# Optimization experiments

Measured on AMD Instinct MI355X. Metric: run time of the kernel, lower is better.

The kernel has to match this reference:

```python
import jax, jax.numpy as jnp
import numpy as np

VOCAB = 50000
D_EMB = 300
N_BINS = 11
B, LQ, LD = 64, 32, 1024
MU = np.array([1.0, 0.9, 0.7, 0.5, 0.3, 0.1, -0.1, -0.3, -0.5, -0.7, -0.9], dtype=np.float32)
SIGMA = np.array([1e-3] + [0.1] * 10, dtype=np.float32)


def setup_inputs() -> dict:
    key = jax.random.key(0)
    ks = jax.random.split(key, 8)
    inputs_q = jax.random.randint(ks[0], (B, LQ), 0, VOCAB, dtype=jnp.int64 if jax.config.jax_enable_x64 else jnp.int32)
    inputs_d = jax.random.randint(ks[1], (B, LD), 0, VOCAB, dtype=jnp.int64 if jax.config.jax_enable_x64 else jnp.int32)
    mask_q = jnp.ones((B, LQ), dtype=jnp.float32)
    mask_d = jnp.ones((B, LD), dtype=jnp.float32)
    word_emb = jax.random.normal(ks[2], (VOCAB, D_EMB), dtype=jnp.float32) * 0.1
    attn_table = jax.random.uniform(ks[3], (VOCAB, 1), dtype=jnp.float32)  # frozen IDF embedding
    idf_w = jax.random.normal(ks[4], (1, 1), dtype=jnp.float32)
    idf_b = jnp.zeros((1,), dtype=jnp.float32)
    dense_w = jax.random.normal(ks[5], (1, N_BINS), dtype=jnp.float32) * 0.1
    dense_b = jnp.zeros((1,), dtype=jnp.float32)
    return {
        'inputs_q': inputs_q, 'inputs_d': inputs_d,
        'mask_q': mask_q, 'mask_d': mask_d,
        'word_emb': word_emb, 'attn_table': attn_table,
        'idf_w': idf_w, 'idf_b': idf_b,
        'dense_w': dense_w, 'dense_b': dense_b,
    }


def _l2_normalize(x, eps=1e-12):
    # matches F.normalize(x, 2, dim=-1): x / max(||x||, eps)
    n = jnp.sqrt(jnp.sum(x * x, axis=-1, keepdims=True))
    return x / jnp.maximum(n, eps)


def reference(inputs_q, inputs_d, mask_q, mask_d, word_emb, attn_table,
              idf_w, idf_b, dense_w, dense_b):
    mu = jnp.asarray(MU)        # [K]
    sigma = jnp.asarray(SIGMA)  # [K]
    # idf attention on query tokens: Linear(1,1) on frozen embedding lookup
    attn_q = attn_table[inputs_q] * idf_w[0, 0] + idf_b[0]          # [B,Lq,1]
    q_embed = _l2_normalize(word_emb[inputs_q])                      # [B,Lq,E]
    d_embed = _l2_normalize(word_emb[inputs_d])                      # [B,Ld,E]
    sim = jnp.einsum('bqe,bde->bqd', q_embed, d_embed)               # [B,Lq,Ld]
    # RBF soft-histogram over n_bins kernels, doc tokens masked
    rbf = jnp.exp(-((sim[..., None] - mu) ** 2) / (sigma ** 2) / 2)  # [B,Lq,Ld,K]
    pooling_sum = jnp.einsum('bqdk,bd->bqk', rbf, mask_d)            # [B,Lq,K]
    wq = mask_q[..., None] * attn_q                                   # [B,Lq,1]
    log_pool = jnp.log(jnp.clip(pooling_sum, 1e-10)) * wq * 0.01     # [B,Lq,K]
    log_pooling_sum = jnp.sum(log_pool, axis=1)                      # [B,K]
    out = jnp.tanh(log_pooling_sum @ dense_w.T + dense_b)            # [B,1]
    return out[:, 0]                                                 # [B]
```

## Files before the change

### kernel.cpp

```cpp
#include <hip/hip_runtime.h>
#include <math.h>

#define VOCAB  50000
#define D_EMB  300
#define NBINS  11
#define BATCH  64
#define LQ     32
#define LD     1024
#define DTILE  64
#define NDT    (LD / DTILE)
#define NSTEP  10
#define FRAG_BLOCK (NSTEP * 512)

typedef __attribute__((ext_vector_type(8))) short short8;
typedef __attribute__((ext_vector_type(4))) float floatx4;

__constant__ float c_mu[NBINS]  = {1.0f, 0.9f, 0.7f, 0.5f, 0.3f, 0.1f,
                                   -0.1f, -0.3f, -0.5f, -0.7f, -0.9f};
__constant__ float c_is2[NBINS] = {500000.0f, 50.f, 50.f, 50.f, 50.f, 50.f,
                                   50.f, 50.f, 50.f, 50.f, 50.f};

static __device__ __forceinline__ unsigned short f32_bf16(float f) {
  unsigned u = __float_as_uint(f);
  u += 0x7FFFu + ((u >> 16) & 1u);
  return (unsigned short)(u >> 16);
}
static __device__ __forceinline__ float bf16_f32(unsigned short h) {
  return __uint_as_float(((unsigned)h) << 16);
}

static __device__ __forceinline__ float stage_rows(
    const float* __restrict__ emb_row,
    short* __restrict__ region,
    int khi, int lane)
{
  const float4* emb4 = (const float4*)emb_row;
  float p = 0.f;
#pragma unroll
  for (int s = 0; s < NSTEP; ++s) {
    const int k0 = 32 * s + 8 * khi;
    float4 fa = make_float4(0.f, 0.f, 0.f, 0.f);
    float4 fb = make_float4(0.f, 0.f, 0.f, 0.f);
    if (k0 < D_EMB)     fa = emb4[k0 >> 2];
    if (k0 + 4 < D_EMB) fb = emb4[(k0 >> 2) + 1];
    unsigned short h[8];
    h[0] = f32_bf16(fa.x); h[1] = f32_bf16(fa.y);
    h[2] = f32_bf16(fa.z); h[3] = f32_bf16(fa.w);
    h[4] = f32_bf16(fb.x); h[5] = f32_bf16(fb.y);
    h[6] = f32_bf16(fb.z); h[7] = f32_bf16(fb.w);
    short8 v;
#pragma unroll
    for (int j = 0; j < 8; ++j) {
      const float x = bf16_f32(h[j]);
      p += x * x;
      v[j] = (short)h[j];
    }
    *(short8*)(region + s * 512 + lane * 8) = v;
  }
  return p;
}

__global__ __launch_bounds__(128) void knrm_prep(
    const int* __restrict__ inputs_q, const float* __restrict__ word_emb,
    short* __restrict__ afrag, float* __restrict__ invq)
{
  const int b    = blockIdx.x;
  const int qt   = threadIdx.x >> 6;
  const int lane = threadIdx.x & 63;
  const int khi  = lane >> 4, rl = lane & 15;
  const int tok  = inputs_q[b * LQ + 16 * qt + rl];
  float p = stage_rows(word_emb + (size_t)tok * D_EMB,
                       afrag + (size_t)(b * 2 + qt) * FRAG_BLOCK, khi, lane);
  p += __shfl_xor(p, 16); p += __shfl_xor(p, 32);
  if (lane < 16) invq[b * LQ + 16 * qt + lane] = 1.f / fmaxf(sqrtf(p), 1e-12f);
}

__global__ __launch_bounds__(256) void knrm_main(
    const int* __restrict__ inputs_d, const float* __restrict__ mask_d,
    const float* __restrict__ word_emb, const short* __restrict__ afrag,
    const float* __restrict__ invq, float* __restrict__ partial)
{
  const int b    = blockIdx.y;
  const int dt   = blockIdx.x;
  const int tid  = threadIdx.x;
  const int wid  = tid >> 6;
  const int lane = tid & 63;
  const int khi  = lane >> 4;
  const int rl   = lane & 15;
  const int qt   = wid >> 1;
  const int dp   = wid & 1;

  __shared__ __align__(16) short Bfrag[4 * FRAG_BLOCK];
  __shared__ float invd_raw[DTILE];
  __shared__ float maskd_s[DTILE];
  __shared__ float red[4][16][NBINS];

  short8 areg[NSTEP];
  {
    const short8* ag = (const short8*)(afrag + (size_t)(b * 2 + qt) * FRAG_BLOCK);
#pragma unroll
    for (int s = 0; s < NSTEP; ++s) areg[s] = ag[s * 64 + lane];
  }
  const float4 iq4 = *(const float4*)&invq[b * LQ + 16 * qt + 4 * khi];

  if (tid < DTILE) maskd_s[tid] = mask_d[b * LD + dt * DTILE + tid];

  {
    const int tok = inputs_d[b * LD + dt * DTILE + 16 * wid + rl];
    float p = stage_rows(word_emb + (size_t)tok * D_EMB,
                         Bfrag + wid * FRAG_BLOCK, khi, lane);
    p += __shfl_xor(p, 16); p += __shfl_xor(p, 32);
    if (lane < 16) invd_raw[16 * wid + lane] = p;
  }
  __syncthreads();

  const short* B0 = Bfrag + (2 * dp) * FRAG_BLOCK;
  const short* B1 = B0 + FRAG_BLOCK;
  floatx4 acc0 = {0.f, 0.f, 0.f, 0.f};
  floatx4 acc1 = {0.f, 0.f, 0.f, 0.f};
#pragma unroll
  for (int s = 0; s < NSTEP; ++s) {
    const short8 b0 = *(const short8*)(B0 + s * 512 + lane * 8);
    const short8 b1 = *(const short8*)(B1 + s * 512 + lane * 8);
    acc0 = __builtin_amdgcn_mfma_f32_16x16x32_bf16(areg[s], b0, acc0, 0, 0, 0);
    acc1 = __builtin_amdgcn_mfma_f32_16x16x32_bf16(areg[s], b1, acc1, 0, 0, 0);
  }

  float ps[4][NBINS];
#pragma unroll
  for (int r = 0; r < 4; ++r)
#pragma unroll
    for (int k = 0; k < NBINS; ++k) ps[r][k] = 0.f;

#pragma unroll
  for (int t = 0; t < 2; ++t) {
    const int   dl = 32 * dp + 16 * t + rl;
    const float id = 1.f / fmaxf(sqrtf(invd_raw[dl]), 1e-12f);
    const float md = maskd_s[dl];
    const floatx4 acc = t ? acc1 : acc0;
#pragma unroll
    for (int r = 0; r < 4; ++r) {
      const float sv = acc[r] * iq4[r] * id;
#pragma unroll
      for (int k = 0; k < NBINS; ++k) {
        const float d = sv - c_mu[k];
        ps[r][k] += md * __expf(-d * d * c_is2[k]);
      }
    }
  }

#pragma unroll
  for (int off = 1; off < 16; off <<= 1)
#pragma unroll
    for (int r = 0; r < 4; ++r)
#pragma unroll
      for (int k = 0; k < NBINS; ++k)
        ps[r][k] += __shfl_xor(ps[r][k], off);

  if (rl == 0)
#pragma unroll
    for (int r = 0; r < 4; ++r)
#pragma unroll
      for (int k = 0; k < NBINS; ++k)
        red[wid][4 * khi + r][k] = ps[r][k];
  __syncthreads();

  for (int v = tid; v < LQ * NBINS; v += 256) {
    const int q = v / NBINS, k = v % NBINS;
    const float sv = (q < 16) ? (red[0][q][k] + red[1][q][k])
                              : (red[2][q - 16][k] + red[3][q - 16][k]);
    partial[((size_t)(b * LQ + q) * NBINS + k) * NDT + dt] = sv;
  }
}

__global__ __launch_bounds__(128) void knrm_finalize(
    const float* __restrict__ partial, const int* __restrict__ inputs_q,
    const float* __restrict__ mask_q, const float* __restrict__ attn_table,
    const float* __restrict__ idf_w, const float* __restrict__ idf_b,
    const float* __restrict__ dense_w, const float* __restrict__ dense_b,
    float* __restrict__ out)
{
  const int b   = blockIdx.x;
  const int tid = threadIdx.x;
  __shared__ float pool[LQ][NBINS];
  __shared__ float wq_s[LQ];
  __shared__ float lps[NBINS];

  for (int v = tid; v < LQ * NBINS; v += 128) {
    const int q = v / NBINS, k = v % NBINS;
    const float* p = partial + ((size_t)(b * LQ + q) * NBINS + k) * NDT;
    float s = 0.f;
#pragma unroll
    for (int t = 0; t < NDT; ++t) s += p[t];
    pool[q][k] = logf(fmaxf(s, 1e-10f));
  }
  if (tid < LQ) {
    const int tok = inputs_q[b * LQ + tid];
    wq_s[tid] = mask_q[b * LQ + tid] * (attn_table[tok] * idf_w[0] + idf_b[0]);
  }
  __syncthreads();
  if (tid < NBINS) {
    float s = 0.f;
    for (int q = 0; q < LQ; ++q) s += pool[q][tid] * wq_s[q];
    lps[tid] = 0.01f * s;
  }
  __syncthreads();
  if (tid == 0) {
    float z = dense_b[0];
    for (int k = 0; k < NBINS; ++k) z += lps[k] * dense_w[k];
    out[b] = tanhf(z);
  }
}

extern "C" void kernel_launch(void* const* d_in, const int* in_sizes, int n_in,
                              void* d_out, int out_size, void* d_ws, size_t ws_size,
                              hipStream_t stream) {
  const int*   inputs_q  = (const int*)d_in[0];
  const int*   inputs_d  = (const int*)d_in[1];
  const float* mask_q    = (const float*)d_in[2];
  const float* mask_d    = (const float*)d_in[3];
  const float* word_emb  = (const float*)d_in[4];
  const float* attn_tab  = (const float*)d_in[5];
  const float* idf_w     = (const float*)d_in[6];
  const float* idf_b     = (const float*)d_in[7];
  const float* dense_w   = (const float*)d_in[8];
  const float* dense_b   = (const float*)d_in[9];
  float* out = (float*)d_out;

  char*  ws      = (char*)d_ws;
  float* partial = (float*)ws;
  short* afrag   = (short*)(ws + (2u << 20));
  float* invq    = (float*)(ws + (4u << 20));

  knrm_prep<<<BATCH, 128, 0, stream>>>(inputs_q, word_emb, afrag, invq);
  dim3 grid(NDT, BATCH);
  knrm_main<<<grid, 256, 0, stream>>>(inputs_d, mask_d, word_emb, afrag, invq, partial);
  knrm_finalize<<<BATCH, 128, 0, stream>>>(partial, inputs_q, mask_q, attn_tab,
                                           idf_w, idf_b, dense_w, dense_b, out);
}
```

Baseline: 138.4 us.

## Precompute bf16 vocabulary table and norms, gather rows directly in main kernel

Adds a kernel that converts the entire embedding table to padded bf16 rows and computes per-row inverse norms, then has the main kernel gather query and document fragments straight from that table into MFMA operands without LDS staging. This removes per-tile fp32 conversion, norm computation and the shared-memory staging barrier. In exchange it converts all vocabulary rows every call, adding a large full-table read and write regardless of which tokens are used.

```diff
diff --git a/kernel.cpp b/kernel.cpp
--- a/kernel.cpp
+++ b/kernel.cpp
@@ -10,7 +10,7 @@
 #define DTILE  64
 #define NDT    (LD / DTILE)
 #define NSTEP  10
-#define FRAG_BLOCK (NSTEP * 512)
+#define KPAD   320
 
 typedef __attribute__((ext_vector_type(8))) short short8;
 typedef __attribute__((ext_vector_type(4))) float floatx4;
@@ -29,56 +29,47 @@
   return __uint_as_float(((unsigned)h) << 16);
 }
 
-static __device__ __forceinline__ float stage_rows(
-    const float* __restrict__ emb_row,
-    short* __restrict__ region,
-    int khi, int lane)
+__global__ __launch_bounds__(256) void knrm_vocab(
+    const float* __restrict__ word_emb, short* __restrict__ emb_bf16,
+    float* __restrict__ invnorm)
 {
-  const float4* emb4 = (const float4*)emb_row;
+  const int row = blockIdx.x * 16 + (threadIdx.x >> 4);
+  const int j   = threadIdx.x & 15;
+  const float4* src = (const float4*)(word_emb + (size_t)row * D_EMB);
+  short* dst = emb_bf16 + (size_t)row * KPAD;
   float p = 0.f;
 #pragma unroll
-  for (int s = 0; s < NSTEP; ++s) {
-    const int k0 = 32 * s + 8 * khi;
-    float4 fa = make_float4(0.f, 0.f, 0.f, 0.f);
-    float4 fb = make_float4(0.f, 0.f, 0.f, 0.f);
-    if (k0 < D_EMB)     fa = emb4[k0 >> 2];
-    if (k0 + 4 < D_EMB) fb = emb4[(k0 >> 2) + 1];
-    unsigned short h[8];
-    h[0] = f32_bf16(fa.x); h[1] = f32_bf16(fa.y);
-    h[2] = f32_bf16(fa.z); h[3] = f32_bf16(fa.w);
-    h[4] = f32_bf16(fb.x); h[5] = f32_bf16(fb.y);
-    h[6] = f32_bf16(fb.z); h[7] = f32_bf16(fb.w);
-    short8 v;
-#pragma unroll
-    for (int j = 0; j < 8; ++j) {
-      const float x = bf16_f32(h[j]);
-      p += x * x;
-      v[j] = (short)h[j];
+  for (int cc = 0; cc < 3; ++cc) {
+    const int c = j + 16 * cc;
+    if (c < 40) {
+      float4 fa = make_float4(0.f, 0.f, 0.f, 0.f);
+      float4 fb = make_float4(0.f, 0.f, 0.f, 0.f);
+      if (8 * c < D_EMB)     fa = src[2 * c];
+      if (8 * c + 4 < D_EMB) fb = src[2 * c + 1];
+      unsigned short h[8];
+      h[0] = f32_bf16(fa.x); h[1] = f32_bf16(fa.y);
+      h[2] = f32_bf16(fa.z); h[3] = f32_bf16(fa.w);
+      h[4] = f32_bf16(fb.x); h[5] = f32_bf16(fb.y);
+      h[6] = f32_bf16(fb.z); h[7] = f32_bf16(fb.w);
+      short8 v;
+#pragma unroll
+      for (int t = 0; t < 8; ++t) {
+        const float x = bf16_f32(h[t]);
+        p += x * x;
+        v[t] = (short)h[t];
+      }
+      *(short8*)(dst + 8 * c) = v;
     }
-    *(short8*)(region + s * 512 + lane * 8) = v;
-  }
-  return p;
-}
-
-__global__ __launch_bounds__(128) void knrm_prep(
-    const int* __restrict__ inputs_q, const float* __restrict__ word_emb,
-    short* __restrict__ afrag, float* __restrict__ invq)
-{
-  const int b    = blockIdx.x;
-  const int qt   = threadIdx.x >> 6;
-  const int lane = threadIdx.x & 63;
-  const int khi  = lane >> 4, rl = lane & 15;
-  const int tok  = inputs_q[b * LQ + 16 * qt + rl];
-  float p = stage_rows(word_emb + (size_t)tok * D_EMB,
-                       afrag + (size_t)(b * 2 + qt) * FRAG_BLOCK, khi, lane);
-  p += __shfl_xor(p, 16); p += __shfl_xor(p, 32);
-  if (lane < 16) invq[b * LQ + 16 * qt + lane] = 1.f / fmaxf(sqrtf(p), 1e-12f);
+  }
+  p += __shfl_xor(p, 1); p += __shfl_xor(p, 2);
+  p += __shfl_xor(p, 4); p += __shfl_xor(p, 8);
+  if (j == 0) invnorm[row] = 1.f / fmaxf(sqrtf(p), 1e-12f);
 }
 
 __global__ __launch_bounds__(256) void knrm_main(
-    const int* __restrict__ inputs_d, const float* __restrict__ mask_d,
-    const float* __restrict__ word_emb, const short* __restrict__ afrag,
-    const float* __restrict__ invq, float* __restrict__ partial)
+    const int* __restrict__ inputs_q, const int* __restrict__ inputs_d,
+    const float* __restrict__ mask_d, const short* __restrict__ emb_bf16,
+    const float* __restrict__ invnorm, float* __restrict__ partial)
 {
   const int b    = blockIdx.y;
   const int dt   = blockIdx.x;
@@ -90,62 +81,46 @@
   const int qt   = wid >> 1;
   const int dp   = wid & 1;
 
-  __shared__ __align__(16) short Bfrag[4 * FRAG_BLOCK];
-  __shared__ float invd_raw[DTILE];
-  __shared__ float maskd_s[DTILE];
   __shared__ float red[4][16][NBINS];
 
-  short8 areg[NSTEP];
-  {
-    const short8* ag = (const short8*)(afrag + (size_t)(b * 2 + qt) * FRAG_BLOCK);
-#pragma unroll
-    for (int s = 0; s < NSTEP; ++s) areg[s] = ag[s * 64 + lane];
-  }
-  const float4 iq4 = *(const float4*)&invq[b * LQ + 16 * qt + 4 * khi];
-
-  if (tid < DTILE) maskd_s[tid] = mask_d[b * LD + dt * DTILE + tid];
-
-  {
-    const int tok = inputs_d[b * LD + dt * DTILE + 16 * wid + rl];
-    float p = stage_rows(word_emb + (size_t)tok * D_EMB,
-                         Bfrag + wid * FRAG_BLOCK, khi, lane);
-    p += __shfl_xor(p, 16); p += __shfl_xor(p, 32);
-    if (lane < 16) invd_raw[16 * wid + lane] = p;
-  }
-  __syncthreads();
-
-  const short* B0 = Bfrag + (2 * dp) * FRAG_BLOCK;
-  const short* B1 = B0 + FRAG_BLOCK;
+  const int dbase = b * LD + dt * DTILE;
+  const int tq  = inputs_q[b * LQ + 16 * qt + rl];
+  const int td0 = inputs_d[dbase + 32 * dp + rl];
+  const int td1 = inputs_d[dbase + 32 * dp + 16 + rl];
+  const short8* arow = (const short8*)(emb_bf16 + (size_t)tq  * KPAD);
+  const short8* b0r  = (const short8*)(emb_bf16 + (size_t)td0 * KPAD);
+  const short8* b1r  = (const short8*)(emb_bf16 + (size_t)td1 * KPAD);
+
   floatx4 acc0 = {0.f, 0.f, 0.f, 0.f};
   floatx4 acc1 = {0.f, 0.f, 0.f, 0.f};
 #pragma unroll
   for (int s = 0; s < NSTEP; ++s) {
-    const short8 b0 = *(const short8*)(B0 + s * 512 + lane * 8);
-    const short8 b1 = *(const short8*)(B1 + s * 512 + lane * 8);
-    acc0 = __builtin_amdgcn_mfma_f32_16x16x32_bf16(areg[s], b0, acc0, 0, 0, 0);
-    acc1 = __builtin_amdgcn_mfma_f32_16x16x32_bf16(areg[s], b1, acc1, 0, 0, 0);
-  }
+    const short8 a  = arow[4 * s + khi];
+    const short8 b0 = b0r [4 * s + khi];
+    const short8 b1 = b1r [4 * s + khi];
+    acc0 = __builtin_amdgcn_mfma_f32_16x16x32_bf16(a, b0, acc0, 0, 0, 0);
+    acc1 = __builtin_amdgcn_mfma_f32_16x16x32_bf16(a, b1, acc1, 0, 0, 0);
+  }
+
+  const float iq_own = invnorm[tq];
+  float iq[4];
+#pragma unroll
+  for (int r = 0; r < 4; ++r) iq[r] = __shfl(iq_own, 4 * khi + r);
+  const float id0 = invnorm[td0], id1 = invnorm[td1];
+  const float md0 = mask_d[dbase + 32 * dp + rl];
+  const float md1 = mask_d[dbase + 32 * dp + 16 + rl];
 
   float ps[4][NBINS];
 #pragma unroll
-  for (int r = 0; r < 4; ++r)
-#pragma unroll
-    for (int k = 0; k < NBINS; ++k) ps[r][k] = 0.f;
-
-#pragma unroll
-  for (int t = 0; t < 2; ++t) {
-    const int   dl = 32 * dp + 16 * t + rl;
-    const float id = 1.f / fmaxf(sqrtf(invd_raw[dl]), 1e-12f);
-    const float md = maskd_s[dl];
-    const floatx4 acc = t ? acc1 : acc0;
-#pragma unroll
-    for (int r = 0; r < 4; ++r) {
-      const float sv = acc[r] * iq4[r] * id;
-#pragma unroll
-      for (int k = 0; k < NBINS; ++k) {
-        const float d = sv - c_mu[k];
-        ps[r][k] += md * __expf(-d * d * c_is2[k]);
-      }
+  for (int r = 0; r < 4; ++r) {
+    const float s0 = acc0[r] * iq[r] * id0;
+    const float s1 = acc1[r] * iq[r] * id1;
+#pragma unroll
+    for (int k = 0; k < NBINS; ++k) {
+      const float d0 = s0 - c_mu[k];
+      const float d1 = s1 - c_mu[k];
+      ps[r][k] = md0 * __expf(-d0 * d0 * c_is2[k])
+               + md1 * __expf(-d1 * d1 * c_is2[k]);
     }
   }
 
@@ -227,14 +202,15 @@
   const float* dense_b   = (const float*)d_in[9];
   float* out = (float*)d_out;
 
-  char*  ws      = (char*)d_ws;
-  float* partial = (float*)ws;
-  short* afrag   = (short*)(ws + (2u << 20));
-  float* invq    = (float*)(ws + (4u << 20));
-
-  knrm_prep<<<BATCH, 128, 0, stream>>>(inputs_q, word_emb, afrag, invq);
+  char*  ws       = (char*)d_ws;
+  float* partial  = (float*)ws;
+  short* emb_bf16 = (short*)(ws + (2u  << 20));
+  float* invnorm  = (float*)(ws + (36u << 20));
+
+  knrm_vocab<<<VOCAB / 16, 256, 0, stream>>>(word_emb, emb_bf16, invnorm);
   dim3 grid(NDT, BATCH);
-  knrm_main<<<grid, 256, 0, stream>>>(inputs_d, mask_d, word_emb, afrag, invq, partial);
+  knrm_main<<<grid, 256, 0, stream>>>(inputs_q, inputs_d, mask_d,
+                                      emb_bf16, invnorm, partial);
   knrm_finalize<<<BATCH, 128, 0, stream>>>(partial, inputs_q, mask_q, attn_tab,
                                            idf_w, idf_b, dense_w, dense_b, out);
 }
```

Measured after the change: 138.0 us. About the same (-0.3%).
